# Optimization experiments

Hardware: AMD Instinct MI355X
Metric: run time of the kernel (lower is better)

Reference implementation:

```python
import jax, jax.numpy as jnp
import numpy as np
from jax import lax

DIM = 192
HEADS = 8
EPS = 1e-5


def setup_inputs() -> dict:
    key = jax.random.key(0)
    ks = jax.random.split(key, 8)
    B, C, H, W = 1, DIM, 64, 64
    x = jax.random.normal(ks[0], (B, C, H, W), dtype=jnp.float32)
    gamma = jnp.ones((C,), dtype=jnp.float32)
    beta = jnp.zeros((C,), dtype=jnp.float32)
    w_qkv = jax.random.normal(ks[1], (3 * C, C), dtype=jnp.float32) * (1.0 / np.sqrt(C))
    # depthwise 3x3 conv: (out_ch=3C, in_ch/groups=1, 3, 3), bias present (Conv2d default)
    w_dw = jax.random.normal(ks[2], (3 * C, 1, 3, 3), dtype=jnp.float32) * (1.0 / 3.0)
    b_dw = jax.random.normal(ks[3], (3 * C,), dtype=jnp.float32) * 0.01
    w_proj = jax.random.normal(ks[4], (C, C), dtype=jnp.float32) * (1.0 / np.sqrt(C))
    temperature = jnp.ones((HEADS, 1, 1), dtype=jnp.float32)
    return {"x": x, "gamma": gamma, "beta": beta, "w_qkv": w_qkv,
            "w_dw": w_dw, "b_dw": b_dw, "w_proj": w_proj,
            "temperature": temperature}


def _mdta(x, gamma, beta, w_qkv, w_dw, b_dw, w_proj, temperature):
    B, C, H, W = x.shape
    heads = HEADS
    d = C // heads
    N = H * W
    # LayerNorm over channel dim (applied on NHWC permute in torch)
    mean = jnp.mean(x, axis=1, keepdims=True)
    var = jnp.var(x, axis=1, keepdims=True)
    x_ln = (x - mean) * lax.rsqrt(var + EPS)
    x_ln = x_ln * gamma[None, :, None, None] + beta[None, :, None, None]
    # 1x1 conv (no bias): [B,3C,H,W]
    qkv = jnp.einsum('oc,bchw->bohw', w_qkv, x_ln)
    # depthwise 3x3 conv, padding=1, groups=3C
    qkv = lax.conv_general_dilated(
        qkv, w_dw, window_strides=(1, 1), padding=((1, 1), (1, 1)),
        dimension_numbers=('NCHW', 'OIHW', 'NCHW'),
        feature_group_count=3 * C)
    qkv = qkv + b_dw[None, :, None, None]
    q, k, v = jnp.split(qkv, 3, axis=1)
    q = q.reshape(B, heads, d, N)
    k = k.reshape(B, heads, d, N)
    v = v.reshape(B, heads, d, N)
    # attn[b,h,n,m] = sum_d q[b,h,d,n] k[b,h,d,m], scaled by learnable temperature
    attn = jnp.einsum('bhdn,bhdm->bhnm', q, k) * temperature  # (heads,1,1) broadcasts
    attn = jax.nn.softmax(attn, axis=-1)
    # out[b,h,d,n] = sum_m attn[b,h,n,m] v[b,h,d,m]
    out = jnp.einsum('bhnm,bhdm->bhdn', attn, v)
    out = out.reshape(B, C, H, W)
    out = jnp.einsum('oc,bchw->bohw', w_proj, out)
    return out + x


def reference(x, gamma, beta, w_qkv, w_dw, b_dw, w_proj, temperature):
    return _mdta(x, gamma, beta, w_qkv, w_dw, b_dw, w_proj, temperature)
```

## Files before the change

kernel.cpp:

```cpp
#include <hip/hip_runtime.h>
#include <hip/hip_bf16.h>


typedef __bf16 bf16;
typedef __bf16 bf16x2 __attribute__((ext_vector_type(2)));
typedef __bf16 bf16x4 __attribute__((ext_vector_type(4)));
typedef __bf16 bf16x8 __attribute__((ext_vector_type(8)));
typedef float f32x4 __attribute__((ext_vector_type(4)));

#define C_DIM 192
#define N_PIX 4096
#define HEADS 8
#define DHEAD 24
#define DPAD 32
#define C3 576
#define NSPLIT 8

__device__ inline float fast_exp2(float x) {
#if __has_builtin(__builtin_amdgcn_exp2f)
    return __builtin_amdgcn_exp2f(x);
#else
    return exp2f(x);
#endif
}

__device__ inline f32x4 mfma16(bf16x8 a, bf16x8 b, f32x4 c) {
    return __builtin_amdgcn_mfma_f32_16x16x32_bf16(a, b, c, 0, 0, 0);
}

__global__ __launch_bounds__(256) void prep_ln(const float* __restrict__ x,
                                               const float* __restrict__ gamma,
                                               const float* __restrict__ beta,
                                               bf16* __restrict__ xln_t,
                                               const float* __restrict__ wqkv,
                                               const float* __restrict__ wproj,
                                               bf16* __restrict__ wqkv_b,
                                               bf16* __restrict__ wproj_b,
                                               float* __restrict__ maxk2) {
    int b = blockIdx.x, t = threadIdx.x;
    if (b >= 256) {
        int idx = (b - 256) * 256 + t;
        if (idx < C3 * C_DIM) wqkv_b[idx] = (bf16)wqkv[idx];
        if (idx < C_DIM * C_DIM) wproj_b[idx] = (bf16)wproj[idx];
        if (b == 256 && t < 8) maxk2[t] = 0.0f;
        return;
    }
    __shared__ float sred[256], ssred[256];
    int pixg = t & 15, cg = t >> 4;
    int p = b * 16 + pixg;
    float v[12];
    float s = 0.f, ss = 0.f;
    for (int j = 0; j < 12; ++j) {
        float f = x[(cg * 12 + j) * N_PIX + p];
        v[j] = f; s += f; ss += f * f;
    }
    sred[t] = s; ssred[t] = ss;
    __syncthreads();
    float S = 0.f, SS = 0.f;
    for (int k = 0; k < 16; ++k) { S += sred[k * 16 + pixg]; SS += ssred[k * 16 + pixg]; }
    float mean = S * (1.0f / C_DIM);
    float var = SS * (1.0f / C_DIM) - mean * mean;
    float rstd = rsqrtf(var + 1e-5f);
    for (int g = 0; g < 3; ++g) {
        bf16x4 w;
        for (int j = 0; j < 4; ++j) {
            int c = cg * 12 + g * 4 + j;
            w[j] = (bf16)((v[g * 4 + j] - mean) * rstd * gamma[c] + beta[c]);
        }
        *(bf16x4*)(xln_t + p * C_DIM + cg * 12 + g * 4) = w;
    }
}

__global__ __launch_bounds__(256) void gemm192(const bf16* __restrict__ A,
                                               const bf16* __restrict__ BT,
                                               bf16* __restrict__ outb) {
    const int K = 192;
    int n0 = blockIdx.x * 64;
    int m0 = blockIdx.y * 64;
    int tid = threadIdx.x;
    int wave = tid >> 6, lane = tid & 63;
    int l16 = lane & 15, quad = lane >> 4;
    int wm = (wave >> 1) * 32, wn = (wave & 1) * 32;
    f32x4 acc[2][2] = {};
    for (int kk = 0; kk < K; kk += 32) {
        bf16x8 a0 = *(const bf16x8*)(A + (m0 + wm + l16) * K + kk + quad * 8);
        bf16x8 a1 = *(const bf16x8*)(A + (m0 + wm + 16 + l16) * K + kk + quad * 8);
        bf16x8 b0 = *(const bf16x8*)(BT + (n0 + wn + l16) * K + kk + quad * 8);
        bf16x8 b1 = *(const bf16x8*)(BT + (n0 + wn + 16 + l16) * K + kk + quad * 8);
        acc[0][0] = mfma16(a0, b0, acc[0][0]);
        acc[0][1] = mfma16(a0, b1, acc[0][1]);
        acc[1][0] = mfma16(a1, b0, acc[1][0]);
        acc[1][1] = mfma16(a1, b1, acc[1][1]);
    }
    for (int i = 0; i < 2; ++i)
        for (int j = 0; j < 2; ++j)
            for (int r = 0; r < 4; ++r) {
                int row = m0 + wm + i * 16 + quad * 4 + r;
                int col = n0 + wn + j * 16 + l16;
                outb[(size_t)row * N_PIX + col] = (bf16)acc[i][j][r];
            }
}

__global__ __launch_bounds__(256) void gemm_proj(const bf16* __restrict__ A,
                                                 const bf16* __restrict__ opart,
                                                 const bf16* __restrict__ lpart,
                                                 float* __restrict__ outf,
                                                 const float* __restrict__ resid) {
    __shared__ __align__(16) bf16 Bld[32 * 200];
    const int K = 192;
    int n0 = blockIdx.x * 32;
    int m0 = blockIdx.y * 64;
    int t = threadIdx.x;
    {
        int h = t >> 5, nl = t & 31;
        int n = n0 + nl;
        float acc[24];
        for (int j = 0; j < 24; ++j) acc[j] = 0.f;
        float l = 0.f;
        for (int s = 0; s < NSPLIT; ++s) {
            const bf16* row = opart + ((size_t)(s * 8 + h) * N_PIX + n) * 24;
            bf16x8 a = *(const bf16x8*)(row);
            bf16x8 b = *(const bf16x8*)(row + 8);
            bf16x8 c = *(const bf16x8*)(row + 16);
            for (int j = 0; j < 8; ++j) {
                acc[j] += (float)a[j];
                acc[8 + j] += (float)b[j];
                acc[16 + j] += (float)c[j];
            }
            l += (float)lpart[(size_t)(s * 8 + h) * N_PIX + n];
        }
        float inv = 1.0f / l;
        bf16* dst = Bld + nl * 200 + h * 24;
        for (int g = 0; g < 3; ++g) {
            bf16x8 w;
            for (int j = 0; j < 8; ++j) w[j] = (bf16)(acc[g * 8 + j] * inv);
            *(bf16x8*)(dst + g * 8) = w;
        }
    }
    __syncthreads();
    int wave = t >> 6, lane = t & 63;
    int l16 = lane & 15, quad = lane >> 4;
    int mrow = m0 + wave * 16;
    float rv[8];
    for (int j = 0; j < 2; ++j)
        for (int r = 0; r < 4; ++r)
            rv[j * 4 + r] = resid[(size_t)(mrow + quad * 4 + r) * N_PIX + n0 + j * 16 + l16];
    f32x4 acc2[2] = {};
    for (int kk = 0; kk < K; kk += 32) {
        bf16x8 a = *(const bf16x8*)(A + (mrow + l16) * K + kk + quad * 8);
        bf16x8 b0 = *(const bf16x8*)(Bld + l16 * 200 + kk + quad * 8);
        bf16x8 b1 = *(const bf16x8*)(Bld + (16 + l16) * 200 + kk + quad * 8);
        acc2[0] = mfma16(a, b0, acc2[0]);
        acc2[1] = mfma16(a, b1, acc2[1]);
    }
    for (int j = 0; j < 2; ++j)
        for (int r = 0; r < 4; ++r) {
            int row = mrow + quad * 4 + r;
            int col = n0 + j * 16 + l16;
            outf[(size_t)row * N_PIX + col] = acc2[j][r] + rv[j * 4 + r];
        }
}

__global__ __launch_bounds__(256) void dwconv(const bf16* __restrict__ qkv,
                                              const float* __restrict__ wdw,
                                              const float* __restrict__ bdw,
                                              bf16* __restrict__ qt,
                                              bf16* __restrict__ kt,
                                              bf16* __restrict__ vl,
                                              float* __restrict__ maxk2) {
    __shared__ float k2s[24][64];
    __shared__ bf16 stg[64 * DPAD];
    int bx = blockIdx.x;
    int part = bx >> 9;
    int h = (bx >> 6) & 7;
    int y = bx & 63;
    int t = threadIdx.x;
    int ch_local = t >> 3;
    int seg = t & 7;
    int px0 = seg * 8;
    bool active = ch_local < 24;

    float acc[8];
    if (active) {
        int ch = part * C_DIM + h * DHEAD + ch_local;
        const bf16* in = qkv + (size_t)ch * N_PIX;
        float w[9];
        for (int i = 0; i < 9; ++i) w[i] = wdw[ch * 9 + i];
        float bias = bdw[ch];
        float rowv[3][10];
        for (int r = 0; r < 3; ++r) {
            int yy = y + r - 1;
            if (yy >= 0 && yy < 64) {
                bf16x8 v8 = *(const bf16x8*)(in + yy * 64 + px0);
                for (int j = 0; j < 8; ++j) rowv[r][j + 1] = (float)v8[j];
                rowv[r][0] = (seg > 0) ? (float)in[yy * 64 + px0 - 1] : 0.f;
                rowv[r][9] = (seg < 7) ? (float)in[yy * 64 + px0 + 8] : 0.f;
            } else {
                for (int j = 0; j < 10; ++j) rowv[r][j] = 0.f;
            }
        }
        for (int j = 0; j < 8; ++j) {
            float a = bias;
            for (int r = 0; r < 3; ++r)
                a += w[r * 3 + 0] * rowv[r][j] + w[r * 3 + 1] * rowv[r][j + 1]
                   + w[r * 3 + 2] * rowv[r][j + 2];
            acc[j] = a;
        }
    }

    if (part == 2) {
        if (active) {
            bf16x8 v8;
            for (int j = 0; j < 8; ++j) v8[j] = (bf16)acc[j];
            *(bf16x8*)(vl + ((size_t)(h * DPAD + ch_local)) * N_PIX + y * 64 + px0) = v8;
        } else {
            int i = t - 192;
            int dd = 24 + (i >> 3);
            int s2 = i & 7;
            bf16 val = (bf16)((dd == 24) ? 1.0f : 0.0f);
            bf16x8 v8;
            for (int j = 0; j < 8; ++j) v8[j] = val;
            *(bf16x8*)(vl + ((size_t)(h * DPAD + dd)) * N_PIX + y * 64 + s2 * 8) = v8;
        }
    } else {
        if (active) {
            for (int j = 0; j < 8; ++j)
                stg[(px0 + j) * DPAD + ch_local] = (bf16)acc[j];
        } else {
            int i = t - 192;
            bf16x8 z;
            for (int j = 0; j < 8; ++j) z[j] = (bf16)0.0f;
            *(bf16x8*)(stg + i * DPAD + 24) = z;
        }
        if (part == 1 && active)
            for (int j = 0; j < 8; ++j) k2s[ch_local][px0 + j] = acc[j] * acc[j];
        __syncthreads();
        bf16* dst = (part == 0 ? qt : kt) + ((size_t)h * N_PIX + y * 64) * DPAD;
        *(bf16x8*)(dst + t * 8) = *(const bf16x8*)(stg + t * 8);
        if (part == 1 && t < 64) {
            float s = 0.f;
            for (int c = 0; c < 24; ++c) s += k2s[c][t];
            for (int off = 1; off < 64; off <<= 1)
                s = fmaxf(s, __shfl_xor(s, off, 64));
            if (t == 0) atomicMax((unsigned int*)(maxk2 + h), __float_as_uint(s));
        }
    }
}

__global__ __launch_bounds__(256, 4) void flash_attn(const bf16* __restrict__ qt,
                                                     const bf16* __restrict__ kt,
                                                     const bf16* __restrict__ vl,
                                                     const float* __restrict__ temp,
                                                     const float* __restrict__ maxk2,
                                                     bf16* __restrict__ opart,
                                                     bf16* __restrict__ lpart) {
    __shared__ __align__(16) bf16 Plds[4 * 1024];

    int tid = threadIdx.x;
    int wave = tid >> 6, lane = tid & 63;
    int l16 = lane & 15, quad = lane >> 4;
    int head = blockIdx.x & 7;
    int qb = (blockIdx.x >> 3) & 15;
    int split = blockIdx.x >> 7;
    int nbase = qb * 256 + wave * 64;
    float tl = temp[head] * 1.44269504f;

    const bf16* qrow = qt + ((size_t)head * N_PIX + nbase) * DPAD;
    bf16x8 aq[4];
    for (int f = 0; f < 4; ++f)
        aq[f] = *(const bf16x8*)(qrow + (size_t)(f * 16 + l16) * DPAD + quad * 8);

    float mk2 = maxk2[head];
    float Bb[4];
    for (int f = 0; f < 4; ++f) {
        float q2 = 0.f;
        for (int j = 0; j < 8; ++j) { float v = (float)aq[f][j]; q2 += v * v; }
        q2 += __shfl_xor(q2, 16, 64);
        q2 += __shfl_xor(q2, 32, 64);
        Bb[f] = fabsf(tl) * sqrtf(q2 * mk2) + 1.0f;
    }

    const bf16* kbase = kt + (size_t)head * N_PIX * DPAD;
    const bf16* vbase = vl + (size_t)head * DPAD * N_PIX;
    bf16* pw = Plds + wave * 1024;

    f32x4 o0[4] = {}, o1[4] = {};

    const int NITER = 64 / NSPLIT;
    int mbase = split * NITER * 64;

    bf16x8 ak[4];
    for (int mt = 0; mt < 4; ++mt)
        ak[mt] = *(const bf16x8*)(kbase + (size_t)(mbase + mt * 16 + l16) * DPAD + quad * 8);

    #pragma unroll 2
    for (int it = 0; it < NITER; ++it) {
        int m0 = mbase + it * 64;
        bf16x8 av0 = *(const bf16x8*)(vbase + (size_t)l16 * N_PIX + m0 + quad * 8);
        bf16x8 av1 = *(const bf16x8*)(vbase + (size_t)(16 + l16) * N_PIX + m0 + quad * 8);
        bf16x8 av2 = *(const bf16x8*)(vbase + (size_t)l16 * N_PIX + m0 + 32 + quad * 8);
        bf16x8 av3 = *(const bf16x8*)(vbase + (size_t)(16 + l16) * N_PIX + m0 + 32 + quad * 8);
        bf16x8 akn[4];
        if (it + 1 < NITER) {
            int m1 = m0 + 64;
            for (int mt = 0; mt < 4; ++mt)
                akn[mt] = *(const bf16x8*)(kbase + (size_t)(m1 + mt * 16 + l16) * DPAD + quad * 8);
        }

        for (int f = 0; f < 4; ++f) {
            f32x4 z = {0.f, 0.f, 0.f, 0.f};
            f32x4 st[4];
            for (int mt = 0; mt < 4; ++mt) st[mt] = mfma16(ak[mt], aq[f], z);
            for (int mt = 0; mt < 4; ++mt) {
                bf16x4 pk;
                for (int r = 0; r < 4; ++r)
                    pk[r] = (bf16)fast_exp2(__builtin_fmaf(st[mt][r], tl, -Bb[f]));
                int chunk = mt * 2 + (quad >> 1);
                *(bf16x4*)(pw + (chunk * 16 + l16) * 8 + (quad & 1) * 4) = pk;
            }
            bf16x8 ap0 = *(const bf16x8*)(pw + (quad * 16 + l16) * 8);
            bf16x8 ap1 = *(const bf16x8*)(pw + ((4 + quad) * 16 + l16) * 8);
            o0[f] = mfma16(av0, ap0, o0[f]);
            o1[f] = mfma16(av1, ap0, o1[f]);
            o0[f] = mfma16(av2, ap1, o0[f]);
            o1[f] = mfma16(av3, ap1, o1[f]);
        }
        if (it + 1 < NITER)
            for (int mt = 0; mt < 4; ++mt) ak[mt] = akn[mt];
    }

    for (int f = 0; f < 4; ++f) {
        int n = nbase + f * 16 + l16;
        size_t rowo = ((size_t)(split * 8 + head) * N_PIX + n) * 24;
        bf16x4 w0;
        for (int r = 0; r < 4; ++r) w0[r] = (bf16)o0[f][r];
        *(bf16x4*)(opart + rowo + quad * 4) = w0;
        if (quad < 2) {
            bf16x4 w1;
            for (int r = 0; r < 4; ++r) w1[r] = (bf16)o1[f][r];
            *(bf16x4*)(opart + rowo + 16 + quad * 4) = w1;
        }
        if (quad == 2)
            lpart[(size_t)(split * 8 + head) * N_PIX + n] = (bf16)o1[f][0];
    }
}

extern "C" void kernel_launch(void* const* d_in, const int* in_sizes, int n_in,
                              void* d_out, int out_size, void* d_ws, size_t ws_size,
                              hipStream_t stream) {
    const float* x     = (const float*)d_in[0];
    const float* gamma = (const float*)d_in[1];
    const float* beta  = (const float*)d_in[2];
    const float* wqkv  = (const float*)d_in[3];
    const float* wdw   = (const float*)d_in[4];
    const float* bdw   = (const float*)d_in[5];
    const float* wproj = (const float*)d_in[6];
    const float* temp  = (const float*)d_in[7];
    float* out = (float*)d_out;

    char* ws = (char*)d_ws;
    bf16* wqkv_b  = (bf16*)(ws + 0);
    bf16* wproj_b = (bf16*)(ws + 221184);
    bf16* xln     = (bf16*)(ws + 294912);
    bf16* qkv     = (bf16*)(ws + 1867776);
    bf16* qt      = (bf16*)(ws + 6586368);
    bf16* kt      = (bf16*)(ws + 8683520);
    bf16* vl      = (bf16*)(ws + 10780672);
    bf16* opart   = (bf16*)(ws + 12877824);
    bf16* lpart   = (bf16*)(ws + 25460736);
    float* maxk2  = (float*)(ws + 25985024);

    prep_ln<<<688, 256, 0, stream>>>(x, gamma, beta, xln, wqkv, wproj, wqkv_b, wproj_b, maxk2);
    gemm192<<<dim3(64, 9), 256, 0, stream>>>(wqkv_b, xln, qkv);
    dwconv<<<1536, 256, 0, stream>>>(qkv, wdw, bdw, qt, kt, vl, maxk2);
    flash_attn<<<NSPLIT * 128, 256, 0, stream>>>(qt, kt, vl, temp, maxk2, opart, lpart);
    gemm_proj<<<dim3(128, 3), 256, 0, stream>>>(wproj_b, opart, lpart, out, x);
}
```

Before: 134.6 us.

## Fuse LayerNorm into QKV GEMM and convert weights to bf16 inline

Removes the separate prep_ln kernel. Each QKV GEMM block now computes LayerNorm for its 64 pixels into shared memory and converts the fp32 weights to bf16 on the fly, and the projection GEMM reads fp32 weights directly. This drops one launch and the xln and bf16-weight workspace round trips. In exchange, LayerNorm is recomputed by all 9 M-blocks per pixel tile, and the fp32 weight loads are wider and scalar-converted inside the K loop.

Result: no change. 132.7 us (-1.4%).

```diff
diff --git a/kernel.cpp b/kernel.cpp
--- a/kernel.cpp
+++ b/kernel.cpp
@@ -28,65 +28,60 @@
     return __builtin_amdgcn_mfma_f32_16x16x32_bf16(a, b, c, 0, 0, 0);
 }
 
-__global__ __launch_bounds__(256) void prep_ln(const float* __restrict__ x,
-                                               const float* __restrict__ gamma,
-                                               const float* __restrict__ beta,
-                                               bf16* __restrict__ xln_t,
-                                               const float* __restrict__ wqkv,
-                                               const float* __restrict__ wproj,
-                                               bf16* __restrict__ wqkv_b,
-                                               bf16* __restrict__ wproj_b,
-                                               float* __restrict__ maxk2) {
-    int b = blockIdx.x, t = threadIdx.x;
-    if (b >= 256) {
-        int idx = (b - 256) * 256 + t;
-        if (idx < C3 * C_DIM) wqkv_b[idx] = (bf16)wqkv[idx];
-        if (idx < C_DIM * C_DIM) wproj_b[idx] = (bf16)wproj[idx];
-        if (b == 256 && t < 8) maxk2[t] = 0.0f;
-        return;
-    }
-    __shared__ float sred[256], ssred[256];
-    int pixg = t & 15, cg = t >> 4;
-    int p = b * 16 + pixg;
-    float v[12];
-    float s = 0.f, ss = 0.f;
-    for (int j = 0; j < 12; ++j) {
-        float f = x[(cg * 12 + j) * N_PIX + p];
-        v[j] = f; s += f; ss += f * f;
-    }
-    sred[t] = s; ssred[t] = ss;
-    __syncthreads();
-    float S = 0.f, SS = 0.f;
-    for (int k = 0; k < 16; ++k) { S += sred[k * 16 + pixg]; SS += ssred[k * 16 + pixg]; }
-    float mean = S * (1.0f / C_DIM);
-    float var = SS * (1.0f / C_DIM) - mean * mean;
-    float rstd = rsqrtf(var + 1e-5f);
-    for (int g = 0; g < 3; ++g) {
-        bf16x4 w;
-        for (int j = 0; j < 4; ++j) {
-            int c = cg * 12 + g * 4 + j;
-            w[j] = (bf16)((v[g * 4 + j] - mean) * rstd * gamma[c] + beta[c]);
-        }
-        *(bf16x4*)(xln_t + p * C_DIM + cg * 12 + g * 4) = w;
-    }
-}
-
-__global__ __launch_bounds__(256) void gemm192(const bf16* __restrict__ A,
-                                               const bf16* __restrict__ BT,
-                                               bf16* __restrict__ outb) {
-    const int K = 192;
+__global__ __launch_bounds__(256) void ln_qkv(const float* __restrict__ x,
+                                              const float* __restrict__ gamma,
+                                              const float* __restrict__ beta,
+                                              const float* __restrict__ wqkv,
+                                              bf16* __restrict__ qkvb,
+                                              float* __restrict__ maxk2) {
+    __shared__ __align__(16) bf16 Bt[64 * 200];
+    __shared__ float gs[C_DIM], bs[C_DIM];
+    const int K = C_DIM;
     int n0 = blockIdx.x * 64;
     int m0 = blockIdx.y * 64;
-    int tid = threadIdx.x;
-    int wave = tid >> 6, lane = tid & 63;
+    int t = threadIdx.x;
+    if (t < C_DIM) { gs[t] = gamma[t]; bs[t] = beta[t]; }
+    if (blockIdx.x == 0 && blockIdx.y == 0 && t < 8) maxk2[t] = 0.0f;
+    __syncthreads();
+
+    int lane = t & 63, wave = t >> 6;
+    {
+        int pl = wave * 16 + (lane & 15);
+        int seg = lane >> 4;
+        int p = n0 + pl;
+        float v[48];
+        float s = 0.f, ss = 0.f;
+        for (int j = 0; j < 48; ++j) {
+            float f = x[(seg * 48 + j) * N_PIX + p];
+            v[j] = f; s += f; ss += f * f;
+        }
+        s += __shfl_xor(s, 16, 64); s += __shfl_xor(s, 32, 64);
+        ss += __shfl_xor(ss, 16, 64); ss += __shfl_xor(ss, 32, 64);
+        float mean = s * (1.0f / C_DIM);
+        float var = ss * (1.0f / C_DIM) - mean * mean;
+        float rstd = rsqrtf(var + 1e-5f);
+        bf16* dst = Bt + pl * 200 + seg * 48;
+        for (int g = 0; g < 6; ++g) {
+            bf16x8 w;
+            for (int j = 0; j < 8; ++j) {
+                int c = seg * 48 + g * 8 + j;
+                w[j] = (bf16)((v[g * 8 + j] - mean) * rstd * gs[c] + bs[c]);
+            }
+            *(bf16x8*)(dst + g * 8) = w;
+        }
+    }
+    __syncthreads();
+
     int l16 = lane & 15, quad = lane >> 4;
     int wm = (wave >> 1) * 32, wn = (wave & 1) * 32;
     f32x4 acc[2][2] = {};
     for (int kk = 0; kk < K; kk += 32) {
-        bf16x8 a0 = *(const bf16x8*)(A + (m0 + wm + l16) * K + kk + quad * 8);
-        bf16x8 a1 = *(const bf16x8*)(A + (m0 + wm + 16 + l16) * K + kk + quad * 8);
-        bf16x8 b0 = *(const bf16x8*)(BT + (n0 + wn + l16) * K + kk + quad * 8);
-        bf16x8 b1 = *(const bf16x8*)(BT + (n0 + wn + 16 + l16) * K + kk + quad * 8);
+        const float* ar0 = wqkv + (m0 + wm + l16) * K + kk + quad * 8;
+        const float* ar1 = wqkv + (m0 + wm + 16 + l16) * K + kk + quad * 8;
+        bf16x8 a0, a1;
+        for (int j = 0; j < 8; ++j) { a0[j] = (bf16)ar0[j]; a1[j] = (bf16)ar1[j]; }
+        bf16x8 b0 = *(const bf16x8*)(Bt + (wn + l16) * 200 + kk + quad * 8);
+        bf16x8 b1 = *(const bf16x8*)(Bt + (wn + 16 + l16) * 200 + kk + quad * 8);
         acc[0][0] = mfma16(a0, b0, acc[0][0]);
         acc[0][1] = mfma16(a0, b1, acc[0][1]);
         acc[1][0] = mfma16(a1, b0, acc[1][0]);
@@ -97,17 +92,201 @@
             for (int r = 0; r < 4; ++r) {
                 int row = m0 + wm + i * 16 + quad * 4 + r;
                 int col = n0 + wn + j * 16 + l16;
-                outb[(size_t)row * N_PIX + col] = (bf16)acc[i][j][r];
-            }
-}
-
-__global__ __launch_bounds__(256) void gemm_proj(const bf16* __restrict__ A,
+                qkvb[(size_t)row * N_PIX + col] = (bf16)acc[i][j][r];
+            }
+}
+
+__global__ __launch_bounds__(256) void dwconv(const bf16* __restrict__ qkv,
+                                              const float* __restrict__ wdw,
+                                              const float* __restrict__ bdw,
+                                              bf16* __restrict__ qt,
+                                              bf16* __restrict__ kt,
+                                              bf16* __restrict__ vl,
+                                              float* __restrict__ maxk2) {
+    __shared__ float k2s[24][64];
+    __shared__ bf16 stg[64 * DPAD];
+    int bx = blockIdx.x;
+    int part = bx >> 9;
+    int h = (bx >> 6) & 7;
+    int y = bx & 63;
+    int t = threadIdx.x;
+    int ch_local = t >> 3;
+    int seg = t & 7;
+    int px0 = seg * 8;
+    bool active = ch_local < 24;
+
+    float acc[8];
+    if (active) {
+        int ch = part * C_DIM + h * DHEAD + ch_local;
+        const bf16* in = qkv + (size_t)ch * N_PIX;
+        float w[9];
+        for (int i = 0; i < 9; ++i) w[i] = wdw[ch * 9 + i];
+        float bias = bdw[ch];
+        float rowv[3][10];
+        for (int r = 0; r < 3; ++r) {
+            int yy = y + r - 1;
+            if (yy >= 0 && yy < 64) {
+                bf16x8 v8 = *(const bf16x8*)(in + yy * 64 + px0);
+                for (int j = 0; j < 8; ++j) rowv[r][j + 1] = (float)v8[j];
+                rowv[r][0] = (seg > 0) ? (float)in[yy * 64 + px0 - 1] : 0.f;
+                rowv[r][9] = (seg < 7) ? (float)in[yy * 64 + px0 + 8] : 0.f;
+            } else {
+                for (int j = 0; j < 10; ++j) rowv[r][j] = 0.f;
+            }
+        }
+        for (int j = 0; j < 8; ++j) {
+            float a = bias;
+            for (int r = 0; r < 3; ++r)
+                a += w[r * 3 + 0] * rowv[r][j] + w[r * 3 + 1] * rowv[r][j + 1]
+                   + w[r * 3 + 2] * rowv[r][j + 2];
+            acc[j] = a;
+        }
+    }
+
+    if (part == 2) {
+        if (active) {
+            bf16x8 v8;
+            for (int j = 0; j < 8; ++j) v8[j] = (bf16)acc[j];
+            *(bf16x8*)(vl + ((size_t)(h * DPAD + ch_local)) * N_PIX + y * 64 + px0) = v8;
+        } else {
+            int i = t - 192;
+            int dd = 24 + (i >> 3);
+            int s2 = i & 7;
+            bf16 val = (bf16)((dd == 24) ? 1.0f : 0.0f);
+            bf16x8 v8;
+            for (int j = 0; j < 8; ++j) v8[j] = val;
+            *(bf16x8*)(vl + ((size_t)(h * DPAD + dd)) * N_PIX + y * 64 + s2 * 8) = v8;
+        }
+    } else {
+        if (active) {
+            for (int j = 0; j < 8; ++j)
+                stg[(px0 + j) * DPAD + ch_local] = (bf16)acc[j];
+        } else {
+            int i = t - 192;
+            bf16x8 z;
+            for (int j = 0; j < 8; ++j) z[j] = (bf16)0.0f;
+            *(bf16x8*)(stg + i * DPAD + 24) = z;
+        }
+        if (part == 1 && active)
+            for (int j = 0; j < 8; ++j) k2s[ch_local][px0 + j] = acc[j] * acc[j];
+        __syncthreads();
+        bf16* dst = (part == 0 ? qt : kt) + ((size_t)h * N_PIX + y * 64) * DPAD;
+        *(bf16x8*)(dst + t * 8) = *(const bf16x8*)(stg + t * 8);
+        if (part == 1 && t < 64) {
+            float s = 0.f;
+            for (int c = 0; c < 24; ++c) s += k2s[c][t];
+            for (int off = 1; off < 64; off <<= 1)
+                s = fmaxf(s, __shfl_xor(s, off, 64));
+            if (t == 0) atomicMax((unsigned int*)(maxk2 + h), __float_as_uint(s));
+        }
+    }
+}
+
+__global__ __launch_bounds__(256, 4) void flash_attn(const bf16* __restrict__ qt,
+                                                     const bf16* __restrict__ kt,
+                                                     const bf16* __restrict__ vl,
+                                                     const float* __restrict__ temp,
+                                                     const float* __restrict__ maxk2,
+                                                     bf16* __restrict__ opart,
+                                                     bf16* __restrict__ lpart) {
+    __shared__ __align__(16) bf16 Plds[4 * 1024];
+
+    int tid = threadIdx.x;
+    int wave = tid >> 6, lane = tid & 63;
+    int l16 = lane & 15, quad = lane >> 4;
+    int head = blockIdx.x & 7;
+    int qb = (blockIdx.x >> 3) & 15;
+    int split = blockIdx.x >> 7;
+    int nbase = qb * 256 + wave * 64;
+    float tl = temp[head] * 1.44269504f;
+
+    const bf16* qrow = qt + ((size_t)head * N_PIX + nbase) * DPAD;
+    bf16x8 aq[4];
+    for (int f = 0; f < 4; ++f)
+        aq[f] = *(const bf16x8*)(qrow + (size_t)(f * 16 + l16) * DPAD + quad * 8);
+
+    float mk2 = maxk2[head];
+    float Bb[4];
+    for (int f = 0; f < 4; ++f) {
+        float q2 = 0.f;
+        for (int j = 0; j < 8; ++j) { float v = (float)aq[f][j]; q2 += v * v; }
+        q2 += __shfl_xor(q2, 16, 64);
+        q2 += __shfl_xor(q2, 32, 64);
+        Bb[f] = fabsf(tl) * sqrtf(q2 * mk2) + 1.0f;
+    }
+
+    const bf16* kbase = kt + (size_t)head * N_PIX * DPAD;
+    const bf16* vbase = vl + (size_t)head * DPAD * N_PIX;
+    bf16* pw = Plds + wave * 1024;
+
+    f32x4 o0[4] = {}, o1[4] = {};
+
+    const int NITER = 64 / NSPLIT;
+    int mbase = split * NITER * 64;
+
+    bf16x8 ak[4];
+    for (int mt = 0; mt < 4; ++mt)
+        ak[mt] = *(const bf16x8*)(kbase + (size_t)(mbase + mt * 16 + l16) * DPAD + quad * 8);
+
+    #pragma unroll 2
+    for (int it = 0; it < NITER; ++it) {
+        int m0 = mbase + it * 64;
+        bf16x8 av0 = *(const bf16x8*)(vbase + (size_t)l16 * N_PIX + m0 + quad * 8);
+        bf16x8 av1 = *(const bf16x8*)(vbase + (size_t)(16 + l16) * N_PIX + m0 + quad * 8);
+        bf16x8 av2 = *(const bf16x8*)(vbase + (size_t)l16 * N_PIX + m0 + 32 + quad * 8);
+        bf16x8 av3 = *(const bf16x8*)(vbase + (size_t)(16 + l16) * N_PIX + m0 + 32 + quad * 8);
+        bf16x8 akn[4];
+        if (it + 1 < NITER) {
+            int m1 = m0 + 64;
+            for (int mt = 0; mt < 4; ++mt)
+                akn[mt] = *(const bf16x8*)(kbase + (size_t)(m1 + mt * 16 + l16) * DPAD + quad * 8);
+        }
+
+        for (int f = 0; f < 4; ++f) {
+            f32x4 z = {0.f, 0.f, 0.f, 0.f};
+            f32x4 st[4];
+            for (int mt = 0; mt < 4; ++mt) st[mt] = mfma16(ak[mt], aq[f], z);
+            for (int mt = 0; mt < 4; ++mt) {
+                bf16x4 pk;
+                for (int r = 0; r < 4; ++r)
+                    pk[r] = (bf16)fast_exp2(__builtin_fmaf(st[mt][r], tl, -Bb[f]));
+                int chunk = mt * 2 + (quad >> 1);
+                *(bf16x4*)(pw + (chunk * 16 + l16) * 8 + (quad & 1) * 4) = pk;
+            }
+            bf16x8 ap0 = *(const bf16x8*)(pw + (quad * 16 + l16) * 8);
+            bf16x8 ap1 = *(const bf16x8*)(pw + ((4 + quad) * 16 + l16) * 8);
+            o0[f] = mfma16(av0, ap0, o0[f]);
+            o1[f] = mfma16(av1, ap0, o1[f]);
+            o0[f] = mfma16(av2, ap1, o0[f]);
+            o1[f] = mfma16(av3, ap1, o1[f]);
+        }
+        if (it + 1 < NITER)
+            for (int mt = 0; mt < 4; ++mt) ak[mt] = akn[mt];
+    }
+
+    for (int f = 0; f < 4; ++f) {
+        int n = nbase + f * 16 + l16;
+        size_t rowo = ((size_t)(split * 8 + head) * N_PIX + n) * 24;
+        bf16x4 w0;
+        for (int r = 0; r < 4; ++r) w0[r] = (bf16)o0[f][r];
+        *(bf16x4*)(opart + rowo + quad * 4) = w0;
+        if (quad < 2) {
+            bf16x4 w1;
+            for (int r = 0; r < 4; ++r) w1[r] = (bf16)o1[f][r];
+            *(bf16x4*)(opart + rowo + 16 + quad * 4) = w1;
+        }
+        if (quad == 2)
+            lpart[(size_t)(split * 8 + head) * N_PIX + n] = (bf16)o1[f][0];
+    }
+}
+
+__global__ __launch_bounds__(256) void gemm_proj(const float* __restrict__ wproj,
                                                  const bf16* __restrict__ opart,
                                                  const bf16* __restrict__ lpart,
                                                  float* __restrict__ outf,
                                                  const float* __restrict__ resid) {
     __shared__ __align__(16) bf16 Bld[32 * 200];
-    const int K = 192;
+    const int K = C_DIM;
     int n0 = blockIdx.x * 32;
     int m0 = blockIdx.y * 64;
     int t = threadIdx.x;
@@ -147,7 +326,9 @@
             rv[j * 4 + r] = resid[(size_t)(mrow + quad * 4 + r) * N_PIX + n0 + j * 16 + l16];
     f32x4 acc2[2] = {};
     for (int kk = 0; kk < K; kk += 32) {
-        bf16x8 a = *(const bf16x8*)(A + (mrow + l16) * K + kk + quad * 8);
+        const float* ar = wproj + (mrow + l16) * K + kk + quad * 8;
+        bf16x8 a;
+        for (int j = 0; j < 8; ++j) a[j] = (bf16)ar[j];
         bf16x8 b0 = *(const bf16x8*)(Bld + l16 * 200 + kk + quad * 8);
         bf16x8 b1 = *(const bf16x8*)(Bld + (16 + l16) * 200 + kk + quad * 8);
         acc2[0] = mfma16(a, b0, acc2[0]);
@@ -159,190 +340,6 @@
             int col = n0 + j * 16 + l16;
             outf[(size_t)row * N_PIX + col] = acc2[j][r] + rv[j * 4 + r];
         }
-}
-
-__global__ __launch_bounds__(256) void dwconv(const bf16* __restrict__ qkv,
-                                              const float* __restrict__ wdw,
-                                              const float* __restrict__ bdw,
-                                              bf16* __restrict__ qt,
-                                              bf16* __restrict__ kt,
-                                              bf16* __restrict__ vl,
-                                              float* __restrict__ maxk2) {
-    __shared__ float k2s[24][64];
-    __shared__ bf16 stg[64 * DPAD];
-    int bx = blockIdx.x;
-    int part = bx >> 9;
-    int h = (bx >> 6) & 7;
-    int y = bx & 63;
-    int t = threadIdx.x;
-    int ch_local = t >> 3;
-    int seg = t & 7;
-    int px0 = seg * 8;
-    bool active = ch_local < 24;
-
-    float acc[8];
-    if (active) {
-        int ch = part * C_DIM + h * DHEAD + ch_local;
-        const bf16* in = qkv + (size_t)ch * N_PIX;
-        float w[9];
-        for (int i = 0; i < 9; ++i) w[i] = wdw[ch * 9 + i];
-        float bias = bdw[ch];
-        float rowv[3][10];
-        for (int r = 0; r < 3; ++r) {
-            int yy = y + r - 1;
-            if (yy >= 0 && yy < 64) {
-                bf16x8 v8 = *(const bf16x8*)(in + yy * 64 + px0);
-                for (int j = 0; j < 8; ++j) rowv[r][j + 1] = (float)v8[j];
-                rowv[r][0] = (seg > 0) ? (float)in[yy * 64 + px0 - 1] : 0.f;
-                rowv[r][9] = (seg < 7) ? (float)in[yy * 64 + px0 + 8] : 0.f;
-            } else {
-                for (int j = 0; j < 10; ++j) rowv[r][j] = 0.f;
-            }
-        }
-        for (int j = 0; j < 8; ++j) {
-            float a = bias;
-            for (int r = 0; r < 3; ++r)
-                a += w[r * 3 + 0] * rowv[r][j] + w[r * 3 + 1] * rowv[r][j + 1]
-                   + w[r * 3 + 2] * rowv[r][j + 2];
-            acc[j] = a;
-        }
-    }
-
-    if (part == 2) {
-        if (active) {
-            bf16x8 v8;
-            for (int j = 0; j < 8; ++j) v8[j] = (bf16)acc[j];
-            *(bf16x8*)(vl + ((size_t)(h * DPAD + ch_local)) * N_PIX + y * 64 + px0) = v8;
-        } else {
-            int i = t - 192;
-            int dd = 24 + (i >> 3);
-            int s2 = i & 7;
-            bf16 val = (bf16)((dd == 24) ? 1.0f : 0.0f);
-            bf16x8 v8;
-            for (int j = 0; j < 8; ++j) v8[j] = val;
-            *(bf16x8*)(vl + ((size_t)(h * DPAD + dd)) * N_PIX + y * 64 + s2 * 8) = v8;
-        }
-    } else {
-        if (active) {
-            for (int j = 0; j < 8; ++j)
-                stg[(px0 + j) * DPAD + ch_local] = (bf16)acc[j];
-        } else {
-            int i = t - 192;
-            bf16x8 z;
-            for (int j = 0; j < 8; ++j) z[j] = (bf16)0.0f;
-            *(bf16x8*)(stg + i * DPAD + 24) = z;
-        }
-        if (part == 1 && active)
-            for (int j = 0; j < 8; ++j) k2s[ch_local][px0 + j] = acc[j] * acc[j];
-        __syncthreads();
-        bf16* dst = (part == 0 ? qt : kt) + ((size_t)h * N_PIX + y * 64) * DPAD;
-        *(bf16x8*)(dst + t * 8) = *(const bf16x8*)(stg + t * 8);
-        if (part == 1 && t < 64) {
-            float s = 0.f;
-            for (int c = 0; c < 24; ++c) s += k2s[c][t];
-            for (int off = 1; off < 64; off <<= 1)
-                s = fmaxf(s, __shfl_xor(s, off, 64));
-            if (t == 0) atomicMax((unsigned int*)(maxk2 + h), __float_as_uint(s));
-        }
-    }
-}
-
-__global__ __launch_bounds__(256, 4) void flash_attn(const bf16* __restrict__ qt,
-                                                     const bf16* __restrict__ kt,
-                                                     const bf16* __restrict__ vl,
-                                                     const float* __restrict__ temp,
-                                                     const float* __restrict__ maxk2,
-                                                     bf16* __restrict__ opart,
-                                                     bf16* __restrict__ lpart) {
-    __shared__ __align__(16) bf16 Plds[4 * 1024];
-
-    int tid = threadIdx.x;
-    int wave = tid >> 6, lane = tid & 63;
-    int l16 = lane & 15, quad = lane >> 4;
-    int head = blockIdx.x & 7;
-    int qb = (blockIdx.x >> 3) & 15;
-    int split = blockIdx.x >> 7;
-    int nbase = qb * 256 + wave * 64;
-    float tl = temp[head] * 1.44269504f;
-
-    const bf16* qrow = qt + ((size_t)head * N_PIX + nbase) * DPAD;
-    bf16x8 aq[4];
-    for (int f = 0; f < 4; ++f)
-        aq[f] = *(const bf16x8*)(qrow + (size_t)(f * 16 + l16) * DPAD + quad * 8);
-
-    float mk2 = maxk2[head];
-    float Bb[4];
-    for (int f = 0; f < 4; ++f) {
-        float q2 = 0.f;
-        for (int j = 0; j < 8; ++j) { float v = (float)aq[f][j]; q2 += v * v; }
-        q2 += __shfl_xor(q2, 16, 64);
-        q2 += __shfl_xor(q2, 32, 64);
-        Bb[f] = fabsf(tl) * sqrtf(q2 * mk2) + 1.0f;
-    }
-
-    const bf16* kbase = kt + (size_t)head * N_PIX * DPAD;
-    const bf16* vbase = vl + (size_t)head * DPAD * N_PIX;
-    bf16* pw = Plds + wave * 1024;
-
-    f32x4 o0[4] = {}, o1[4] = {};
-
-    const int NITER = 64 / NSPLIT;
-    int mbase = split * NITER * 64;
-
-    bf16x8 ak[4];
-    for (int mt = 0; mt < 4; ++mt)
-        ak[mt] = *(const bf16x8*)(kbase + (size_t)(mbase + mt * 16 + l16) * DPAD + quad * 8);
-
-    #pragma unroll 2
-    for (int it = 0; it < NITER; ++it) {
-        int m0 = mbase + it * 64;
-        bf16x8 av0 = *(const bf16x8*)(vbase + (size_t)l16 * N_PIX + m0 + quad * 8);
-        bf16x8 av1 = *(const bf16x8*)(vbase + (size_t)(16 + l16) * N_PIX + m0 + quad * 8);
-        bf16x8 av2 = *(const bf16x8*)(vbase + (size_t)l16 * N_PIX + m0 + 32 + quad * 8);
-        bf16x8 av3 = *(const bf16x8*)(vbase + (size_t)(16 + l16) * N_PIX + m0 + 32 + quad * 8);
-        bf16x8 akn[4];
-        if (it + 1 < NITER) {
-            int m1 = m0 + 64;
-            for (int mt = 0; mt < 4; ++mt)
-                akn[mt] = *(const bf16x8*)(kbase + (size_t)(m1 + mt * 16 + l16) * DPAD + quad * 8);
-        }
-
-        for (int f = 0; f < 4; ++f) {
-            f32x4 z = {0.f, 0.f, 0.f, 0.f};
-            f32x4 st[4];
-            for (int mt = 0; mt < 4; ++mt) st[mt] = mfma16(ak[mt], aq[f], z);
-            for (int mt = 0; mt < 4; ++mt) {
-                bf16x4 pk;
-                for (int r = 0; r < 4; ++r)
-                    pk[r] = (bf16)fast_exp2(__builtin_fmaf(st[mt][r], tl, -Bb[f]));
-                int chunk = mt * 2 + (quad >> 1);
-                *(bf16x4*)(pw + (chunk * 16 + l16) * 8 + (quad & 1) * 4) = pk;
-            }
-            bf16x8 ap0 = *(const bf16x8*)(pw + (quad * 16 + l16) * 8);
-            bf16x8 ap1 = *(const bf16x8*)(pw + ((4 + quad) * 16 + l16) * 8);
-            o0[f] = mfma16(av0, ap0, o0[f]);
-            o1[f] = mfma16(av1, ap0, o1[f]);
-            o0[f] = mfma16(av2, ap1, o0[f]);
-            o1[f] = mfma16(av3, ap1, o1[f]);
-        }
-        if (it + 1 < NITER)
-            for (int mt = 0; mt < 4; ++mt) ak[mt] = akn[mt];
-    }
-
-    for (int f = 0; f < 4; ++f) {
-        int n = nbase + f * 16 + l16;
-        size_t rowo = ((size_t)(split * 8 + head) * N_PIX + n) * 24;
-        bf16x4 w0;
-        for (int r = 0; r < 4; ++r) w0[r] = (bf16)o0[f][r];
-        *(bf16x4*)(opart + rowo + quad * 4) = w0;
-        if (quad < 2) {
-            bf16x4 w1;
-            for (int r = 0; r < 4; ++r) w1[r] = (bf16)o1[f][r];
-            *(bf16x4*)(opart + rowo + 16 + quad * 4) = w1;
-        }
-        if (quad == 2)
-            lpart[(size_t)(split * 8 + head) * N_PIX + n] = (bf16)o1[f][0];
-    }
 }
 
 extern "C" void kernel_launch(void* const* d_in, const int* in_sizes, int n_in,
@@ -359,20 +356,16 @@
     float* out = (float*)d_out;
 
     char* ws = (char*)d_ws;
-    bf16* wqkv_b  = (bf16*)(ws + 0);
-    bf16* wproj_b = (bf16*)(ws + 221184);
-    bf16* xln     = (bf16*)(ws + 294912);
-    bf16* qkv     = (bf16*)(ws + 1867776);
-    bf16* qt      = (bf16*)(ws + 6586368);
-    bf16* kt      = (bf16*)(ws + 8683520);
-    bf16* vl      = (bf16*)(ws + 10780672);
-    bf16* opart   = (bf16*)(ws + 12877824);
-    bf16* lpart   = (bf16*)(ws + 25460736);
-    float* maxk2  = (float*)(ws + 25985024);
-
-    prep_ln<<<688, 256, 0, stream>>>(x, gamma, beta, xln, wqkv, wproj, wqkv_b, wproj_b, maxk2);
-    gemm192<<<dim3(64, 9), 256, 0, stream>>>(wqkv_b, xln, qkv);
+    bf16* qkv     = (bf16*)(ws + 0);
+    bf16* qt      = (bf16*)(ws + 4718592);
+    bf16* kt      = (bf16*)(ws + 6815744);
+    bf16* vl      = (bf16*)(ws + 8912896);
+    bf16* opart   = (bf16*)(ws + 11010048);
+    bf16* lpart   = (bf16*)(ws + 23592960);
+    float* maxk2  = (float*)(ws + 24117248);
+
+    ln_qkv<<<dim3(64, 9), 256, 0, stream>>>(x, gamma, beta, wqkv, qkv, maxk2);
     dwconv<<<1536, 256, 0, stream>>>(qkv, wdw, bdw, qt, kt, vl, maxk2);
     flash_attn<<<NSPLIT * 128, 256, 0, stream>>>(qt, kt, vl, temp, maxk2, opart, lpart);
-    gemm_proj<<<dim3(128, 3), 256, 0, stream>>>(wproj_b, opart, lpart, out, x);
-}
+    gemm_proj<<<dim3(128, 3), 256, 0, stream>>>(wproj, opart, lpart, out, x);
+}
```
